# Optimization experiments

Measured on AMD Instinct MI355X. Metric: run time of the kernel, lower is better.

The kernel has to match this reference:

```python
import jax, jax.numpy as jnp
import numpy as np

N = 16000        # nodes
E = 256000       # edges
D_IN = 1280      # input node features
HID = 256        # hidden dim (all hidden_dims equal; required by res_linear shapes)
HEADS = 8
C = HID // HEADS # 32 channels per head
G = 32           # graphs in the batch
O = 64           # output labels (GO terms)
NB = 2           # conv blocks = len(hidden_dims) - 1
EPS = 1e-5


def _bn(h, g, b):
    # eval-mode BatchNorm1d with running_mean=0, running_var=1 (init state)
    return h * (g / jnp.sqrt(1.0 + EPS)) + b


def _seg_softmax(logits, seg, num):
    # numerically-stable segment softmax (PyG softmax semantics)
    m = jax.ops.segment_max(logits, seg, num_segments=num)
    e = jnp.exp(logits - m[seg])
    s = jax.ops.segment_sum(e, seg, num_segments=num)
    return e / (s[seg] + 1e-16)


def setup_inputs() -> dict:
    key = jax.random.key(0)
    ks = jax.random.split(key, 16)
    w = lambda i, sh: jax.random.normal(ks[i], sh, jnp.float32) * 0.05
    return {
        "x": jax.random.normal(ks[0], (N, D_IN), jnp.float32),
        "edge_index": jax.random.randint(ks[1], (2, E), 0, N),
        "batch": jnp.sort(jax.random.randint(ks[2], (N,), 0, G)),
        # feature_proj: Linear -> ReLU -> BN
        "fp_W": w(3, (D_IN, HID)), "fp_b": jnp.zeros(HID),
        "fp_g": jnp.ones(HID), "fp_be": jnp.zeros(HID),
        # GATv2Conv per block: lin_l, lin_r, att, out-bias
        "gat_Wl": w(4, (NB, HID, HID)), "gat_bl": jnp.zeros((NB, HID)),
        "gat_Wr": w(5, (NB, HID, HID)), "gat_br": jnp.zeros((NB, HID)),
        "gat_att": w(6, (NB, HEADS, C)), "gat_bias": jnp.zeros((NB, HID)),
        # GINConv MLP: Linear -> ReLU -> BN
        "gin_W": w(7, (NB, HID, HID)), "gin_b": jnp.zeros((NB, HID)),
        "gin_g": jnp.ones((NB, HID)), "gin_be": jnp.zeros((NB, HID)),
        # PyG LayerNorm (graph mode) affine
        "ln_g": jnp.ones((NB, HID)), "ln_b": jnp.zeros((NB, HID)),
        # residual linears
        "res_W": w(8, (NB, HID, HID)), "res_b": jnp.zeros((NB, HID)),
        # GlobalAttention gate MLP
        "pool_W1": w(9, (HID, HID)), "pool_b1": jnp.zeros(HID),
        "pool_W2": w(10, (HID, 1)), "pool_b2": jnp.zeros(1),
        # O label heads (hierarchy=None -> just the MLP), stacked
        "head_W1": w(11, (O, HID, 256)), "head_b1": jnp.zeros((O, 256)),
        "head_g": jnp.ones((O, 256)), "head_be": jnp.zeros((O, 256)),
        "head_W2": w(12, (O, 256)), "head_b2": jnp.zeros(O),
    }


def reference(x, edge_index, batch, fp_W, fp_b, fp_g, fp_be,
              gat_Wl, gat_bl, gat_Wr, gat_br, gat_att, gat_bias,
              gin_W, gin_b, gin_g, gin_be, ln_g, ln_b, res_W, res_b,
              pool_W1, pool_b1, pool_W2, pool_b2,
              head_W1, head_b1, head_g, head_be, head_W2, head_b2):
    n = x.shape[0]
    # feature_proj (eval: dropout = identity)
    h = _bn(jax.nn.relu(x @ fp_W + fp_b), fp_g, fp_be)

    src0, dst0 = edge_index[0], edge_index[1]
    loop = jnp.arange(n)
    src = jnp.concatenate([src0, loop])  # GATv2 adds self-loops by default
    dst = jnp.concatenate([dst0, loop])

    for i in range(NB):
        # ---- GATv2Conv (no activation after, per original control flow) ----
        xl = (h @ gat_Wl[i] + gat_bl[i]).reshape(n, HEADS, C)
        xr = (h @ gat_Wr[i] + gat_br[i]).reshape(n, HEADS, C)
        msg = xl[src]                                   # [E', H, C]
        eact = jax.nn.leaky_relu(msg + xr[dst], 0.2)
        logit = jnp.einsum('ehc,hc->eh', eact, gat_att[i])
        alpha = _seg_softmax(logit, dst, n)             # [E', H]
        h = jax.ops.segment_sum(alpha[:, :, None] * msg, dst,
                                num_segments=n).reshape(n, HID) + gat_bias[i]
        # ---- GINConv: nn((1+0)*x + sum_neighbors), then leaky_relu ----
        agg = jax.ops.segment_sum(h[src0], dst0, num_segments=n)
        gin = _bn(jax.nn.relu((h + agg) @ gin_W[i] + gin_b[i]), gin_g[i], gin_be[i])
        h = jax.nn.leaky_relu(gin, 0.2)
        # ---- PyG LayerNorm (graph mode, batch=None: global mean/std) + residual ----
        mu = h.mean()
        sd = jnp.std(h)
        ln = (h - mu) / (sd + EPS) * ln_g[i] + ln_b[i]
        h = jax.nn.leaky_relu(ln + (h @ res_W[i] + res_b[i]), 0.2)

    # ---- GlobalAttention pooling ----
    gate = jnp.tanh(h @ pool_W1 + pool_b1) @ pool_W2 + pool_b2   # [N, 1]
    a = _seg_softmax(gate[:, 0], batch, G)
    emb = jax.ops.segment_sum(a[:, None] * h, batch, num_segments=G)  # [G, HID]

    # ---- O label heads (hierarchy None -> MLP only), vectorized ----
    z = jnp.einsum('bd,odh->boh', emb, head_W1) + head_b1[None]
    z = _bn(jax.nn.silu(z), head_g[None], head_be[None])
    out = jnp.einsum('boh,oh->bo', z, head_W2) + head_b2[None]
    return out[:, :, None]  # torch.stack(outputs, dim=1) -> [G, O, 1]
```

## Files before the change

### kernel.cpp

```cpp
#include <hip/hip_runtime.h>
#include <math.h>

#define N_NODES 16000
#define N_EDGES 256000
#define EPE (N_EDGES + N_NODES)
#define DIN 1280
#define HID 256
#define HEADS 8
#define CPH 32
#define NG 32
#define NO 64
#define EPSC 1e-5f
#define CAP 32
#define XPAD 264
#define SPAD 40

typedef __bf16 bf16;
typedef __attribute__((ext_vector_type(8))) __bf16 bf16x8;
typedef __attribute__((ext_vector_type(4))) float floatx4;

__device__ __forceinline__ float lrelu(float v) { return v > 0.f ? v : 0.2f * v; }
__device__ __forceinline__ float bflo(unsigned int u) { return __uint_as_float(u << 16); }
__device__ __forceinline__ float bfhi(unsigned int u) { return __uint_as_float(u & 0xffff0000u); }

__global__ void wconv_gen(const float* __restrict__ W, bf16* __restrict__ Wt, int K, int total) {
    int idx = blockIdx.x * 256 + threadIdx.x;
    if (idx >= total) return;
    int per = K * HID;
    int l = idx / per, rem = idx - l * per;
    int n = rem / K, k = rem - n * K;
    Wt[idx] = (bf16)W[(size_t)l * per + (size_t)k * HID + n];
}

__global__ void wconv_pair(const float* __restrict__ Wl, const float* __restrict__ Wr,
                           bf16* __restrict__ Wt) {
    int idx = blockIdx.x * 256 + threadIdx.x;
    int n = idx >> 8, k = idx & 255;
    float v = (n < 256) ? Wl[(size_t)k * HID + n] : Wr[(size_t)k * HID + (n - 256)];
    Wt[idx] = (bf16)v;
}

__global__ __launch_bounds__(256) void gemm64(
    const bf16* __restrict__ A, const bf16* __restrict__ Bt,
    const float* __restrict__ bias, const float* __restrict__ bias2,
    bf16* __restrict__ C, int K, int ldc, int mode,
    const float* __restrict__ g, const float* __restrict__ be)
{
    __shared__ __align__(16) bf16 As[2][64 * SPAD];
    __shared__ __align__(16) bf16 Bs[2][64 * SPAD];
    const int tid = threadIdx.x;
    const int bm = blockIdx.y * 64, bn = blockIdx.x * 64;
    const int w = tid >> 6, lane = tid & 63;
    const int wm = w * 16;
    const int lrow = lane & 15, lk8 = (lane >> 4) * 8;
    const int row = tid >> 2, k8 = (tid & 3) * 8;

    const bf16* gA = A + (size_t)(bm + row) * K + k8;
    const bf16* gB = Bt + (size_t)(bn + row) * K + k8;

    floatx4 acc[4];
#pragma unroll
    for (int j = 0; j < 4; j++) acc[j] = (floatx4){0.f, 0.f, 0.f, 0.f};

    const int nk = K >> 5;
    bf16x8 ra = *(const bf16x8*)gA;
    bf16x8 rb = *(const bf16x8*)gB;

    for (int it = 0; it < nk; ++it) {
        int p = it & 1;
        *(bf16x8*)&As[p][row * SPAD + k8] = ra;
        *(bf16x8*)&Bs[p][row * SPAD + k8] = rb;
        __syncthreads();
        if (it + 1 < nk) {
            ra = *(const bf16x8*)(gA + (it + 1) * 32);
            rb = *(const bf16x8*)(gB + (it + 1) * 32);
        }
        bf16x8 af = *(const bf16x8*)&As[p][(wm + lrow) * SPAD + lk8];
        bf16x8 bfr[4];
#pragma unroll
        for (int j = 0; j < 4; j++) bfr[j] = *(const bf16x8*)&Bs[p][(16 * j + lrow) * SPAD + lk8];
#pragma unroll
        for (int j = 0; j < 4; j++)
            acc[j] = __builtin_amdgcn_mfma_f32_16x16x32_bf16(af, bfr[j], acc[j], 0, 0, 0);
    }

    const float inv = rsqrtf(1.f + EPSC);
    const int row0 = bm + wm + (lane >> 4) * 4;
#pragma unroll
    for (int j = 0; j < 4; j++) {
        int col = bn + 16 * j + lrow;
        float bcol = (col < HID) ? bias[col] : bias2[col - HID];
        float gc = (mode >= 1) ? g[col] * inv : 0.f;
        float bec = (mode >= 1) ? be[col] : 0.f;
#pragma unroll
        for (int r = 0; r < 4; r++) {
            float z = acc[j][r] + bcol;
            if (mode >= 1) { z = fmaxf(z, 0.f); z = z * gc + bec; }
            if (mode == 2) z = lrelu(z);
            C[(size_t)(row0 + r) * ldc + col] = (bf16)z;
        }
    }
}

__global__ __launch_bounds__(256, 1) void gemm_f32A(
    const float* __restrict__ A, const bf16* __restrict__ Bt,
    const float* __restrict__ bias, bf16* __restrict__ C, int K,
    const float* __restrict__ g, const float* __restrict__ be)
{
    __shared__ __align__(16) bf16 As[2][128 * SPAD];
    __shared__ __align__(16) bf16 Bs[2][128 * SPAD];
    const int tid = threadIdx.x;
    const int bm = blockIdx.y * 128, bn = blockIdx.x * 128;
    const int w = tid >> 6, lane = tid & 63;
    const int wm = (w & 1) * 64, wn = (w >> 1) * 64;
    const int lrow = lane & 15, lk8 = (lane >> 4) * 8;

    floatx4 acc[4][4];
#pragma unroll
    for (int i = 0; i < 4; i++)
#pragma unroll
        for (int j = 0; j < 4; j++) acc[i][j] = (floatx4){0.f, 0.f, 0.f, 0.f};

    const int r2 = tid >> 1, c2 = tid & 1;
    const float* gA = A + (size_t)(bm + r2) * K + c2 * 16;
    const bf16* gB = Bt + (size_t)(bn + r2) * K + c2 * 16;
    bf16* sA = &As[0][r2 * SPAD + c2 * 16];
    bf16* sB = &Bs[0][r2 * SPAD + c2 * 16];

    const int nk = K >> 5;
    float4 a[4][4];
    bf16x8 b[4][2];
#pragma unroll
    for (int u = 0; u < 4; u++) {
        const float* pa = gA + u * 32;
        a[u][0] = *(const float4*)(pa + 0);
        a[u][1] = *(const float4*)(pa + 4);
        a[u][2] = *(const float4*)(pa + 8);
        a[u][3] = *(const float4*)(pa + 12);
        const bf16* pb = gB + u * 32;
        b[u][0] = *(const bf16x8*)(pb + 0);
        b[u][1] = *(const bf16x8*)(pb + 8);
    }

    for (int it0 = 0; it0 < nk; it0 += 4) {
#pragma unroll
        for (int u = 0; u < 4; u++) {
            const int it = it0 + u;
            const int p = u & 1;
            const int po = p * 128 * SPAD;
            bf16x8 h0, h1;
            h0[0] = (bf16)a[u][0].x; h0[1] = (bf16)a[u][0].y; h0[2] = (bf16)a[u][0].z; h0[3] = (bf16)a[u][0].w;
            h0[4] = (bf16)a[u][1].x; h0[5] = (bf16)a[u][1].y; h0[6] = (bf16)a[u][1].z; h0[7] = (bf16)a[u][1].w;
            h1[0] = (bf16)a[u][2].x; h1[1] = (bf16)a[u][2].y; h1[2] = (bf16)a[u][2].z; h1[3] = (bf16)a[u][2].w;
            h1[4] = (bf16)a[u][3].x; h1[5] = (bf16)a[u][3].y; h1[6] = (bf16)a[u][3].z; h1[7] = (bf16)a[u][3].w;
            *(bf16x8*)(sA + po + 0) = h0;
            *(bf16x8*)(sA + po + 8) = h1;
            *(bf16x8*)(sB + po + 0) = b[u][0];
            *(bf16x8*)(sB + po + 8) = b[u][1];
            __syncthreads();
            if (it + 4 < nk) {
                const float* pa = gA + (it + 4) * 32;
                a[u][0] = *(const float4*)(pa + 0);
                a[u][1] = *(const float4*)(pa + 4);
                a[u][2] = *(const float4*)(pa + 8);
                a[u][3] = *(const float4*)(pa + 12);
                const bf16* pb = gB + (it + 4) * 32;
                b[u][0] = *(const bf16x8*)(pb + 0);
                b[u][1] = *(const bf16x8*)(pb + 8);
            }
            bf16x8 af[4], bfr[4];
#pragma unroll
            for (int i = 0; i < 4; i++) af[i] = *(const bf16x8*)&As[p][(wm + 16 * i + lrow) * SPAD + lk8];
#pragma unroll
            for (int j = 0; j < 4; j++) bfr[j] = *(const bf16x8*)&Bs[p][(wn + 16 * j + lrow) * SPAD + lk8];
#pragma unroll
            for (int i = 0; i < 4; i++)
#pragma unroll
                for (int j = 0; j < 4; j++)
                    acc[i][j] = __builtin_amdgcn_mfma_f32_16x16x32_bf16(af[i], bfr[j], acc[i][j], 0, 0, 0);
        }
    }

    const float inv = rsqrtf(1.f + EPSC);
#pragma unroll
    for (int j = 0; j < 4; j++) {
        int col = bn + wn + 16 * j + lrow;
        float bcol = bias[col];
        float gc = g[col] * inv;
        float bec = be[col];
#pragma unroll
        for (int i = 0; i < 4; i++) {
            int row0 = bm + wm + 16 * i + (lane >> 4) * 4;
#pragma unroll
            for (int r = 0; r < 4; r++) {
                float z = fmaxf(acc[i][j][r] + bcol, 0.f) * gc + bec;
                C[(size_t)(row0 + r) * HID + col] = (bf16)z;
            }
        }
    }
}

__global__ void hist_kernel(const int* __restrict__ ei, int* __restrict__ cnt) {
    int e = blockIdx.x * 256 + threadIdx.x;
    if (e >= EPE) return;
    int d = (e < N_EDGES) ? ei[N_EDGES + e] : (e - N_EDGES);
    atomicAdd(&cnt[d], 1);
}

__global__ __launch_bounds__(1024) void scan_kernel(const int* __restrict__ cnt,
                                                    int* __restrict__ roff, int* __restrict__ cursor) {
    __shared__ int wsum[16];
    int t = threadIdx.x;
    int base = t * 16;
    int local[16]; int s = 0;
#pragma unroll
    for (int i = 0; i < 16; i++) {
        int idx = base + i;
        int v = (idx < N_NODES) ? cnt[idx] : 0;
        local[i] = s; s += v;
    }
    int lane = t & 63, wid = t >> 6;
    int incl = s;
    for (int o = 1; o < 64; o <<= 1) { int v = __shfl_up(incl, o); if (lane >= o) incl += v; }
    if (lane == 63) wsum[wid] = incl;
    __syncthreads();
    if (t == 0) { int a = 0; for (int k = 0; k < 16; k++) { int v = wsum[k]; wsum[k] = a; a += v; } }
    __syncthreads();
    int texcl = incl - s + wsum[wid];
#pragma unroll
    for (int i = 0; i < 16; i++) {
        int idx = base + i;
        if (idx < N_NODES) { int o = texcl + local[i]; roff[idx] = o; cursor[idx] = o; }
    }
    if (t == 1023) roff[N_NODES] = texcl + s;
}

__global__ void scatter_kernel(const int* __restrict__ ei, int* __restrict__ cursor,
                               int* __restrict__ esrc) {
    int e = blockIdx.x * 256 + threadIdx.x;
    if (e >= EPE) return;
    int s, d;
    if (e < N_EDGES) { s = ei[e]; d = ei[N_EDGES + e]; }
    else { s = d = e - N_EDGES; }
    int pos = atomicAdd(&cursor[d], 1);
    esrc[pos] = s;
}

__global__ __launch_bounds__(256) void gat_fused(
    const bf16* __restrict__ XLR, const int* __restrict__ roff, const int* __restrict__ esrc,
    const float* __restrict__ att, const float* __restrict__ gbias, bf16* __restrict__ out)
{
    const int d = blockIdx.x, t = threadIdx.x;
    const int beg = roff[d], deg = roff[d + 1] - beg;
    __shared__ __align__(16) bf16 xs[CAP][XPAD];
    __shared__ __align__(16) float4 xa4[8 * 16];
    __shared__ float llog[CAP * 8];
    __shared__ float m_s[8], s_s[8], resc[8];

    if (t < 128) {
        int hh = t >> 4, cc = t & 15;
        int c = hh * 32 + cc * 2;
        float xr0 = (float)XLR[(size_t)d * 512 + 256 + c];
        float xr1 = (float)XLR[(size_t)d * 512 + 256 + c + 1];
        xa4[hh * 16 + cc] = (float4){xr0, att[c], xr1, att[c + 1]};
    }
    if (t < 8) { m_s[t] = -INFINITY; s_s[t] = 0.f; }

    const int jj = t & 31;
    const int hh = t >> 5;
    const int g = t >> 5, l = t & 31;
    float acc = 0.f;

    for (int c0 = 0; c0 < deg; c0 += CAP) {
        int cn = min(CAP, deg - c0);
        __syncthreads();
        for (int r = g; r < cn; r += 8) {
            int s = esrc[beg + c0 + r];
            *(bf16x8*)(&xs[r][l * 8]) = *(const bf16x8*)(XLR + (size_t)s * 512 + l * 8);
        }
        __syncthreads();
        if (jj < cn) {
            float lg = 0.f;
#pragma unroll
            for (int cc = 0; cc < 16; cc++) {
                int ce = (cc + jj) & 15;
                unsigned int p = *(const unsigned int*)&xs[jj][hh * 32 + ce * 2];
                float4 xa = xa4[hh * 16 + ce];
                lg += lrelu(bflo(p) + xa.x) * xa.y + lrelu(bfhi(p) + xa.z) * xa.w;
            }
            llog[jj * 8 + hh] = lg;
        }
        __syncthreads();
        if (t < 64) {
            int h2 = t & 7, j0 = t >> 3;
            float mx = -INFINITY;
            for (int j = j0; j < cn; j += 8) mx = fmaxf(mx, llog[j * 8 + h2]);
            for (int o = 8; o < 64; o <<= 1) mx = fmaxf(mx, __shfl_xor(mx, o));
            float mo = m_s[h2];
            float mn = fmaxf(mo, mx);
            float ss = 0.f;
            for (int j = j0; j < cn; j += 8) {
                float e = __expf(llog[j * 8 + h2] - mn);
                llog[j * 8 + h2] = e;
                ss += e;
            }
            for (int o = 8; o < 64; o <<= 1) ss += __shfl_xor(ss, o);
            if (t < 8) {
                float r = __expf(mo - mn);
                resc[h2] = r;
                s_s[h2] = s_s[h2] * r + ss;
                m_s[h2] = mn;
            }
        }
        __syncthreads();
        acc *= resc[hh];
        for (int j = 0; j < cn; j++)
            acc += llog[j * 8 + hh] * (float)xs[j][t];
    }
    out[(size_t)d * HID + t] = (bf16)(gbias[t] + acc / (s_s[hh] + 1e-16f));
}

__global__ __launch_bounds__(256) void gin_gather(
    const unsigned int* __restrict__ hu, const int* __restrict__ roff,
    const int* __restrict__ esrc, unsigned int* __restrict__ uu)
{
    int d = blockIdx.x, t = threadIdx.x;
    int grp = t >> 7, c = t & 127;
    int beg = roff[d], end = roff[d + 1];
    float a0 = 0.f, a1 = 0.f;
    int p = beg + grp;
    while (p + 14 < end) {
        int s[8];
#pragma unroll
        for (int k = 0; k < 8; k++) s[k] = esrc[p + 2 * k];
        unsigned int v[8];
#pragma unroll
        for (int k = 0; k < 8; k++) v[k] = hu[(size_t)s[k] * 128 + c];
#pragma unroll
        for (int k = 0; k < 8; k++) { a0 += bflo(v[k]); a1 += bfhi(v[k]); }
        p += 16;
    }
    for (; p < end; p += 2) {
        unsigned int v = hu[(size_t)esrc[p] * 128 + c];
        a0 += bflo(v); a1 += bfhi(v);
    }
    __shared__ float plo[128], phi[128];
    if (grp) { plo[c] = a0; phi[c] = a1; }
    __syncthreads();
    if (!grp) {
        a0 += plo[c]; a1 += phi[c];
        bf16 b0 = (bf16)a0, b1 = (bf16)a1;
        unsigned int r = ((unsigned int)*(unsigned short*)&b0) |
                         (((unsigned int)*(unsigned short*)&b1) << 16);
        uu[(size_t)d * 128 + c] = r;
    }
}

__global__ void stats_kernel(const bf16* __restrict__ x, float2* __restrict__ part, int n8) {
    float s = 0.f, sq = 0.f;
    for (int i = blockIdx.x * blockDim.x + threadIdx.x; i < n8; i += gridDim.x * blockDim.x) {
        bf16x8 v = *(const bf16x8*)(x + (size_t)i * 8);
#pragma unroll
        for (int j = 0; j < 8; j++) { float f = (float)v[j]; s += f; sq += f * f; }
    }
    for (int o = 32; o > 0; o >>= 1) { s += __shfl_down(s, o); sq += __shfl_down(sq, o); }
    __shared__ float ls[4], lq[4];
    int wid = threadIdx.x >> 6, lane = threadIdx.x & 63;
    if (lane == 0) { ls[wid] = s; lq[wid] = sq; }
    __syncthreads();
    if (threadIdx.x == 0)
        part[blockIdx.x] = make_float2(ls[0] + ls[1] + ls[2] + ls[3],
                                       lq[0] + lq[1] + lq[2] + lq[3]);
}

__global__ void stats_reduce(const float2* __restrict__ part, float* __restrict__ stat) {
    int t = threadIdx.x;
    float2 v = part[t];
    float s = v.x, q = v.y;
    for (int o = 32; o > 0; o >>= 1) { s += __shfl_down(s, o); q += __shfl_down(q, o); }
    __shared__ float ls[4], lq[4];
    int wid = t >> 6, lane = t & 63;
    if (lane == 0) { ls[wid] = s; lq[wid] = q; }
    __syncthreads();
    if (t == 0) { stat[0] = ls[0] + ls[1] + ls[2] + ls[3]; stat[1] = lq[0] + lq[1] + lq[2] + lq[3]; }
}

__global__ void ln_res_kernel(const bf16* __restrict__ h, const bf16* __restrict__ r,
                              const float* __restrict__ stats, const float* __restrict__ g,
                              const float* __restrict__ b, bf16* __restrict__ out)
{
    int i = (blockIdx.x * 256 + threadIdx.x) * 4;
    const float inv_n = 1.f / (float)((size_t)N_NODES * HID);
    float mu = stats[0] * inv_n;
    float var = stats[1] * inv_n - mu * mu;
    float sd = sqrtf(fmaxf(var, 0.f));
    float rs = 1.f / (sd + EPSC);
    int ch = i & (HID - 1);
#pragma unroll
    for (int j = 0; j < 4; j++) {
        float v = ((float)h[i + j] - mu) * rs * g[ch + j] + b[ch + j] + (float)r[i + j];
        out[i + j] = (bf16)lrelu(v);
    }
}

__global__ void gbound_kernel(const int* __restrict__ batch, int* __restrict__ gstart) {
    int g = threadIdx.x;
    if (g > NG) return;
    int lo = 0, hi = N_NODES;
    while (lo < hi) { int mid = (lo + hi) >> 1; if (batch[mid] < g) lo = mid + 1; else hi = mid; }
    gstart[g] = lo;
}

__global__ __launch_bounds__(256) void pool_gate_kernel(const bf16* __restrict__ t,
    const float* __restrict__ W2, const float* __restrict__ b2, float* __restrict__ gate)
{
    int n = blockIdx.x * 4 + (threadIdx.x >> 6);
    int lane = threadIdx.x & 63;
    const bf16* p = t + (size_t)n * HID + lane * 4;
    float4 w = *(const float4*)(W2 + lane * 4);
    float s = tanhf((float)p[0]) * w.x + tanhf((float)p[1]) * w.y
            + tanhf((float)p[2]) * w.z + tanhf((float)p[3]) * w.w;
    for (int o = 32; o > 0; o >>= 1) s += __shfl_down(s, o);
    if (lane == 0) gate[n] = s + b2[0];
}

__global__ __launch_bounds__(256) void pool_stats_kernel(
    float* __restrict__ gate, const int* __restrict__ gstart)
{
    int g = blockIdx.x, t = threadIdx.x;
    int lo = gstart[g], hi = gstart[g + 1];
    __shared__ float red[256];
    float m = -INFINITY;
    for (int n = lo + t; n < hi; n += 256) m = fmaxf(m, gate[n]);
    red[t] = m; __syncthreads();
    for (int st = 128; st > 0; st >>= 1) { if (t < st) red[t] = fmaxf(red[t], red[t + st]); __syncthreads(); }
    m = red[0]; __syncthreads();
    float s = 0.f;
    for (int n = lo + t; n < hi; n += 256) s += __expf(gate[n] - m);
    red[t] = s; __syncthreads();
    for (int st = 128; st > 0; st >>= 1) { if (t < st) red[t] += red[t + st]; __syncthreads(); }
    float sinv = 1.f / (red[0] + 1e-16f);
    for (int n = lo + t; n < hi; n += 256) gate[n] = __expf(gate[n] - m) * sinv;
}

__global__ __launch_bounds__(256) void emb_accum_kernel(
    const float* __restrict__ a, const int* __restrict__ batch,
    const bf16* __restrict__ h, float* __restrict__ emb)
{
    int n0 = blockIdx.x * 32, t = threadIdx.x;
    int cur = batch[n0]; float acc = 0.f;
    for (int j = 0; j < 32; j++) {
        int n = n0 + j;
        int b = batch[n];
        if (b != cur) { atomicAdd(&emb[cur * HID + t], acc); cur = b; acc = 0.f; }
        acc += a[n] * (float)h[(size_t)n * HID + t];
    }
    atomicAdd(&emb[cur * HID + t], acc);
}

__global__ __launch_bounds__(256) void heads_kernel(
    const float* __restrict__ emb, const float* __restrict__ W1, const float* __restrict__ b1,
    const float* __restrict__ hg, const float* __restrict__ hbe, const float* __restrict__ W2,
    const float* __restrict__ b2, float* __restrict__ out)
{
    int o = blockIdx.x;
    int g0 = blockIdx.y * 4;
    int k = threadIdx.x;
    __shared__ float se[4][HID];
    __shared__ float red[256];
#pragma unroll
    for (int j = 0; j < 4; j++) se[j][k] = emb[(g0 + j) * HID + k];
    __syncthreads();
    const float* w1p = W1 + (size_t)o * HID * HID + k;
    float zb = b1[o * HID + k];
    float z0 = zb, z1 = zb, z2 = zb, z3 = zb;
#pragma unroll 8
    for (int d = 0; d < HID; d++) {
        float w = w1p[(size_t)d * HID];
        z0 = fmaf(se[0][d], w, z0);
        z1 = fmaf(se[1][d], w, z1);
        z2 = fmaf(se[2][d], w, z2);
        z3 = fmaf(se[3][d], w, z3);
    }
    const float gk = hg[o * HID + k] * rsqrtf(1.f + EPSC);
    const float bek = hbe[o * HID + k];
    const float w2 = W2[o * HID + k];
    const float b2o = b2[o];
    float zz[4] = {z0, z1, z2, z3};
#pragma unroll
    for (int j = 0; j < 4; j++) {
        float z = zz[j];
        float sil = z / (1.f + expf(-z));
        red[k] = (sil * gk + bek) * w2;
        __syncthreads();
        for (int st = 128; st > 0; st >>= 1) { if (k < st) red[k] += red[k + st]; __syncthreads(); }
        if (k == 0) out[(g0 + j) * NO + o] = red[0] + b2o;
        __syncthreads();
    }
}

extern "C" void kernel_launch(void* const* d_in, const int* in_sizes, int n_in,
                              void* d_out, int out_size, void* d_ws, size_t ws_size,
                              hipStream_t stream) {
    const float* x        = (const float*)d_in[0];
    const int*   ei       = (const int*)  d_in[1];
    const int*   batch    = (const int*)  d_in[2];
    const float* fp_W     = (const float*)d_in[3];
    const float* fp_b     = (const float*)d_in[4];
    const float* fp_g     = (const float*)d_in[5];
    const float* fp_be    = (const float*)d_in[6];
    const float* gat_Wl   = (const float*)d_in[7];
    const float* gat_bl   = (const float*)d_in[8];
    const float* gat_Wr   = (const float*)d_in[9];
    const float* gat_br   = (const float*)d_in[10];
    const float* gat_att  = (const float*)d_in[11];
    const float* gat_bias = (const float*)d_in[12];
    const float* gin_W    = (const float*)d_in[13];
    const float* gin_b    = (const float*)d_in[14];
    const float* gin_g    = (const float*)d_in[15];
    const float* gin_be   = (const float*)d_in[16];
    const float* ln_g     = (const float*)d_in[17];
    const float* ln_b     = (const float*)d_in[18];
    const float* res_W    = (const float*)d_in[19];
    const float* res_b    = (const float*)d_in[20];
    const float* pool_W1  = (const float*)d_in[21];
    const float* pool_b1  = (const float*)d_in[22];
    const float* pool_W2  = (const float*)d_in[23];
    const float* pool_b2  = (const float*)d_in[24];
    const float* head_W1  = (const float*)d_in[25];
    const float* head_b1  = (const float*)d_in[26];
    const float* head_g   = (const float*)d_in[27];
    const float* head_be  = (const float*)d_in[28];
    const float* head_W2  = (const float*)d_in[29];
    const float* head_b2  = (const float*)d_in[30];
    float* out = (float*)d_out;

    char* base = (char*)d_ws;
    size_t off = 0;
    auto alloc = [&](size_t bytes) -> char* {
        char* p = base + off; off += (bytes + 255) & ~(size_t)255; return p;
    };
    int*   esrc   = (int*)  alloc((size_t)EPE * 4);
    int*   cnt    = (int*)  alloc((size_t)N_NODES * 4);
    int*   roff   = (int*)  alloc((size_t)(N_NODES + 1) * 4);
    int*   cursor = (int*)  alloc((size_t)N_NODES * 4);
    float* gate   = (float*)alloc((size_t)N_NODES * 4);
    int*   gstart = (int*)  alloc((NG + 1) * 4);
    float* emb    = (float*)alloc(NG * HID * 4);
    float* stat   = (float*)alloc(8);
    float2* statp = (float2*)alloc(256 * 8);
    bf16*  Hb0    = (bf16*) alloc((size_t)N_NODES * HID * 2);
    bf16*  Hb1    = (bf16*) alloc((size_t)N_NODES * HID * 2);
    bf16*  XLR    = (bf16*) alloc((size_t)N_NODES * 512 * 2);
    bf16*  fpWt   = (bf16*) alloc((size_t)DIN * HID * 2);
    bf16*  wlrT0  = (bf16*) alloc((size_t)512 * HID * 2);
    bf16*  wlrT1  = (bf16*) alloc((size_t)512 * HID * 2);
    bf16*  gwT    = (bf16*) alloc((size_t)2 * HID * HID * 2);
    bf16*  rwT    = (bf16*) alloc((size_t)2 * HID * HID * 2);
    bf16*  pwT    = (bf16*) alloc((size_t)HID * HID * 2);
    bf16*  Ub     = XLR;
    bf16*  wlrT[2] = { wlrT0, wlrT1 };

    wconv_gen<<<(DIN * HID + 255) / 256, 256, 0, stream>>>(fp_W, fpWt, DIN, DIN * HID);
    wconv_pair<<<512, 256, 0, stream>>>(gat_Wl, gat_Wr, wlrT0);
    wconv_pair<<<512, 256, 0, stream>>>(gat_Wl + HID * HID, gat_Wr + HID * HID, wlrT1);
    wconv_gen<<<512, 256, 0, stream>>>(gin_W, gwT, HID, 2 * HID * HID);
    wconv_gen<<<512, 256, 0, stream>>>(res_W, rwT, HID, 2 * HID * HID);
    wconv_gen<<<256, 256, 0, stream>>>(pool_W1, pwT, HID, HID * HID);

    hipMemsetAsync(cnt, 0, N_NODES * sizeof(int), stream);
    hist_kernel<<<(EPE + 255) / 256, 256, 0, stream>>>(ei, cnt);
    scan_kernel<<<1, 1024, 0, stream>>>(cnt, roff, cursor);
    scatter_kernel<<<(EPE + 255) / 256, 256, 0, stream>>>(ei, cursor, esrc);
    gbound_kernel<<<1, 64, 0, stream>>>(batch, gstart);

    dim3 gridF(2, 125);
    dim3 g64_256(4, 250);
    dim3 g64_512(8, 250);
    gemm_f32A<<<gridF, 256, 0, stream>>>(x, fpWt, fp_b, Hb0, DIN, fp_g, fp_be);

    for (int i = 0; i < 2; i++) {
        gemm64<<<g64_512, 256, 0, stream>>>(Hb0, wlrT[i], gat_bl + i * HID, gat_br + i * HID,
                                            XLR, HID, 512, 0, nullptr, nullptr);
        gat_fused<<<N_NODES, 256, 0, stream>>>(XLR, roff, esrc, gat_att + i * HEADS * CPH,
                                               gat_bias + i * HID, Hb1);
        gin_gather<<<N_NODES, 256, 0, stream>>>((const unsigned int*)Hb1, roff, esrc,
                                                (unsigned int*)Ub);
        gemm64<<<g64_256, 256, 0, stream>>>(Ub, gwT + (size_t)i * HID * HID, gin_b + i * HID,
                                            nullptr, Hb0, HID, HID, 2,
                                            gin_g + i * HID, gin_be + i * HID);
        stats_kernel<<<256, 256, 0, stream>>>(Hb0, statp, (N_NODES * HID) / 8);
        stats_reduce<<<1, 256, 0, stream>>>(statp, stat);
        gemm64<<<g64_256, 256, 0, stream>>>(Hb0, rwT + (size_t)i * HID * HID, res_b + i * HID,
                                            nullptr, Hb1, HID, HID, 0, nullptr, nullptr);
        ln_res_kernel<<<(N_NODES * HID) / 1024, 256, 0, stream>>>(Hb0, Hb1, stat,
                                                                  ln_g + i * HID, ln_b + i * HID, Hb0);
    }

    gemm64<<<g64_256, 256, 0, stream>>>(Hb0, pwT, pool_b1, nullptr, Hb1, HID, HID, 0, nullptr, nullptr);
    pool_gate_kernel<<<N_NODES / 4, 256, 0, stream>>>(Hb1, pool_W2, pool_b2, gate);
    pool_stats_kernel<<<NG, 256, 0, stream>>>(gate, gstart);
    hipMemsetAsync(emb, 0, NG * HID * sizeof(float), stream);
    emb_accum_kernel<<<N_NODES / 32, 256, 0, stream>>>(gate, batch, Hb0, emb);

    dim3 hgrid(NO, 8);
    heads_kernel<<<hgrid, 256, 0, stream>>>(emb, head_W1, head_b1, head_g, head_be,
                                            head_W2, head_b2, out);
}
```

Before: 608.4 us.

## Fuse LayerNorm stats and residual epilogue into GEMMs, rework GAT aggregation

```diff
diff --git a/kernel.cpp b/kernel.cpp
--- a/kernel.cpp
+++ b/kernel.cpp
@@ -22,6 +22,10 @@
 __device__ __forceinline__ float lrelu(float v) { return v > 0.f ? v : 0.2f * v; }
 __device__ __forceinline__ float bflo(unsigned int u) { return __uint_as_float(u << 16); }
 __device__ __forceinline__ float bfhi(unsigned int u) { return __uint_as_float(u & 0xffff0000u); }
+__device__ __forceinline__ unsigned int bfpack(float x, float y) {
+    bf16 b0 = (bf16)x, b1 = (bf16)y;
+    return ((unsigned int)*(unsigned short*)&b0) | (((unsigned int)*(unsigned short*)&b1) << 16);
+}
 
 __global__ void wconv_gen(const float* __restrict__ W, bf16* __restrict__ Wt, int K, int total) {
     int idx = blockIdx.x * 256 + threadIdx.x;
@@ -44,7 +48,8 @@
     const bf16* __restrict__ A, const bf16* __restrict__ Bt,
     const float* __restrict__ bias, const float* __restrict__ bias2,
     bf16* __restrict__ C, int K, int ldc, int mode,
-    const float* __restrict__ g, const float* __restrict__ be)
+    const float* __restrict__ g, const float* __restrict__ be,
+    float2* __restrict__ statp, const float* __restrict__ stat)
 {
     __shared__ __align__(16) bf16 As[2][64 * SPAD];
     __shared__ __align__(16) bf16 Bs[2][64 * SPAD];
@@ -86,19 +91,46 @@
 
     const float inv = rsqrtf(1.f + EPSC);
     const int row0 = bm + wm + (lane >> 4) * 4;
+    float mu = 0.f, rs = 0.f;
+    if (mode == 3) {
+        const float inv_n = 1.f / (float)((size_t)N_NODES * HID);
+        mu = stat[0] * inv_n;
+        float var = stat[1] * inv_n - mu * mu;
+        rs = 1.f / (sqrtf(fmaxf(var, 0.f)) + EPSC);
+    }
+    float sz = 0.f, sq = 0.f;
 #pragma unroll
     for (int j = 0; j < 4; j++) {
         int col = bn + 16 * j + lrow;
         float bcol = (col < HID) ? bias[col] : bias2[col - HID];
-        float gc = (mode >= 1) ? g[col] * inv : 0.f;
-        float bec = (mode >= 1) ? be[col] : 0.f;
+        float gc = (mode >= 2) ? g[col] : 0.f;
+        float bec = (mode >= 2) ? be[col] : 0.f;
 #pragma unroll
         for (int r = 0; r < 4; r++) {
             float z = acc[j][r] + bcol;
-            if (mode >= 1) { z = fmaxf(z, 0.f); z = z * gc + bec; }
-            if (mode == 2) z = lrelu(z);
+            if (mode == 2) {
+                z = fmaxf(z, 0.f) * (gc * inv) + bec;
+                z = lrelu(z);
+                sz += z; sq += z * z;
+            } else if (mode == 3) {
+                float h = (float)A[(size_t)(row0 + r) * K + col];
+                z = (h - mu) * rs * gc + bec + z;
+                z = lrelu(z);
+            }
             C[(size_t)(row0 + r) * ldc + col] = (bf16)z;
         }
+    }
+    if (mode == 2) {
+        for (int o = 32; o > 0; o >>= 1) { sz += __shfl_down(sz, o); sq += __shfl_down(sq, o); }
+        __syncthreads();
+        float* rs_ = (float*)&As[0][0];
+        float* rq_ = (float*)&Bs[0][0];
+        if (lane == 0) { rs_[w] = sz; rq_[w] = sq; }
+        __syncthreads();
+        if (tid == 0)
+            statp[blockIdx.y * gridDim.x + blockIdx.x] =
+                make_float2(rs_[0] + rs_[1] + rs_[2] + rs_[3],
+                            rq_[0] + rq_[1] + rq_[2] + rq_[3]);
     }
 }
 
@@ -208,7 +240,9 @@
 }
 
 __global__ __launch_bounds__(1024) void scan_kernel(const int* __restrict__ cnt,
-                                                    int* __restrict__ roff, int* __restrict__ cursor) {
+                                                    int* __restrict__ roff, int* __restrict__ cursor,
+                                                    const int* __restrict__ batch,
+                                                    int* __restrict__ gstart) {
     __shared__ int wsum[16];
     int t = threadIdx.x;
     int base = t * 16;
@@ -233,6 +267,11 @@
         if (idx < N_NODES) { int o = texcl + local[i]; roff[idx] = o; cursor[idx] = o; }
     }
     if (t == 1023) roff[N_NODES] = texcl + s;
+    if (t <= NG) {
+        int lo = 0, hi = N_NODES;
+        while (lo < hi) { int mid = (lo + hi) >> 1; if (batch[mid] < t) lo = mid + 1; else hi = mid; }
+        gstart[t] = lo;
+    }
 }
 
 __global__ void scatter_kernel(const int* __restrict__ ei, int* __restrict__ cursor,
@@ -255,6 +294,7 @@
     __shared__ __align__(16) bf16 xs[CAP][XPAD];
     __shared__ __align__(16) float4 xa4[8 * 16];
     __shared__ float llog[CAP * 8];
+    __shared__ float comb[256];
     __shared__ float m_s[8], s_s[8], resc[8];
 
     if (t < 128) {
@@ -268,15 +308,19 @@
 
     const int jj = t & 31;
     const int hh = t >> 5;
-    const int g = t >> 5, l = t & 31;
-    float acc = 0.f;
+    const int sg = t >> 5, sl = t & 31;
+    const int half = t >> 7;
+    const int tc = t & 127;
+    const int ch0 = tc * 2;
+    const int ha = tc >> 4;
+    float a0 = 0.f, a1 = 0.f;
 
     for (int c0 = 0; c0 < deg; c0 += CAP) {
         int cn = min(CAP, deg - c0);
         __syncthreads();
-        for (int r = g; r < cn; r += 8) {
+        for (int r = sg; r < cn; r += 8) {
             int s = esrc[beg + c0 + r];
-            *(bf16x8*)(&xs[r][l * 8]) = *(const bf16x8*)(XLR + (size_t)s * 512 + l * 8);
+            *(bf16x8*)(&xs[r][sl * 8]) = *(const bf16x8*)(XLR + (size_t)s * 512 + sl * 8);
         }
         __syncthreads();
         if (jj < cn) {
@@ -313,11 +357,24 @@
             }
         }
         __syncthreads();
-        acc *= resc[hh];
-        for (int j = 0; j < cn; j++)
-            acc += llog[j * 8 + hh] * (float)xs[j][t];
-    }
-    out[(size_t)d * HID + t] = (bf16)(gbias[t] + acc / (s_s[hh] + 1e-16f));
+        float rsf = resc[ha];
+        a0 *= rsf; a1 *= rsf;
+        for (int j = half; j < cn; j += 2) {
+            float wgt = llog[j * 8 + ha];
+            unsigned int p = *(const unsigned int*)&xs[j][ch0];
+            a0 = fmaf(wgt, bflo(p), a0);
+            a1 = fmaf(wgt, bfhi(p), a1);
+        }
+    }
+    __syncthreads();
+    if (half) { comb[ch0] = a0; comb[ch0 + 1] = a1; }
+    __syncthreads();
+    if (!half) {
+        float r = 1.f / (s_s[ha] + 1e-16f);
+        float v0 = gbias[ch0] + (a0 + comb[ch0]) * r;
+        float v1 = gbias[ch0 + 1] + (a1 + comb[ch0 + 1]) * r;
+        *(unsigned int*)(out + (size_t)d * HID + ch0) = bfpack(v0, v1);
+    }
 }
 
 __global__ __launch_bounds__(256) void gin_gather(
@@ -349,66 +406,20 @@
     __syncthreads();
     if (!grp) {
         a0 += plo[c]; a1 += phi[c];
-        bf16 b0 = (bf16)a0, b1 = (bf16)a1;
-        unsigned int r = ((unsigned int)*(unsigned short*)&b0) |
-                         (((unsigned int)*(unsigned short*)&b1) << 16);
-        uu[(size_t)d * 128 + c] = r;
-    }
-}
-
-__global__ void stats_kernel(const bf16* __restrict__ x, float2* __restrict__ part, int n8) {
-    float s = 0.f, sq = 0.f;
-    for (int i = blockIdx.x * blockDim.x + threadIdx.x; i < n8; i += gridDim.x * blockDim.x) {
-        bf16x8 v = *(const bf16x8*)(x + (size_t)i * 8);
-#pragma unroll
-        for (int j = 0; j < 8; j++) { float f = (float)v[j]; s += f; sq += f * f; }
-    }
-    for (int o = 32; o > 0; o >>= 1) { s += __shfl_down(s, o); sq += __shfl_down(sq, o); }
-    __shared__ float ls[4], lq[4];
-    int wid = threadIdx.x >> 6, lane = threadIdx.x & 63;
-    if (lane == 0) { ls[wid] = s; lq[wid] = sq; }
-    __syncthreads();
-    if (threadIdx.x == 0)
-        part[blockIdx.x] = make_float2(ls[0] + ls[1] + ls[2] + ls[3],
-                                       lq[0] + lq[1] + lq[2] + lq[3]);
-}
-
-__global__ void stats_reduce(const float2* __restrict__ part, float* __restrict__ stat) {
+        uu[(size_t)d * 128 + c] = bfpack(a0, a1);
+    }
+}
+
+__global__ void stats_reduce(const float2* __restrict__ part, float* __restrict__ stat, int n) {
     int t = threadIdx.x;
-    float2 v = part[t];
-    float s = v.x, q = v.y;
+    float s = 0.f, q = 0.f;
+    for (int i = t; i < n; i += 256) { float2 v = part[i]; s += v.x; q += v.y; }
     for (int o = 32; o > 0; o >>= 1) { s += __shfl_down(s, o); q += __shfl_down(q, o); }
     __shared__ float ls[4], lq[4];
     int wid = t >> 6, lane = t & 63;
     if (lane == 0) { ls[wid] = s; lq[wid] = q; }
     __syncthreads();
     if (t == 0) { stat[0] = ls[0] + ls[1] + ls[2] + ls[3]; stat[1] = lq[0] + lq[1] + lq[2] + lq[3]; }
-}
-
-__global__ void ln_res_kernel(const bf16* __restrict__ h, const bf16* __restrict__ r,
-                              const float* __restrict__ stats, const float* __restrict__ g,
-                              const float* __restrict__ b, bf16* __restrict__ out)
-{
-    int i = (blockIdx.x * 256 + threadIdx.x) * 4;
-    const float inv_n = 1.f / (float)((size_t)N_NODES * HID);
-    float mu = stats[0] * inv_n;
-    float var = stats[1] * inv_n - mu * mu;
-    float sd = sqrtf(fmaxf(var, 0.f));
-    float rs = 1.f / (sd + EPSC);
-    int ch = i & (HID - 1);
-#pragma unroll
-    for (int j = 0; j < 4; j++) {
-        float v = ((float)h[i + j] - mu) * rs * g[ch + j] + b[ch + j] + (float)r[i + j];
-        out[i + j] = (bf16)lrelu(v);
-    }
-}
-
-__global__ void gbound_kernel(const int* __restrict__ batch, int* __restrict__ gstart) {
-    int g = threadIdx.x;
-    if (g > NG) return;
-    int lo = 0, hi = N_NODES;
-    while (lo < hi) { int mid = (lo + hi) >> 1; if (batch[mid] < g) lo = mid + 1; else hi = mid; }
-    gstart[g] = lo;
 }
 
 __global__ __launch_bounds__(256) void pool_gate_kernel(const bf16* __restrict__ t,
@@ -548,7 +559,7 @@
     int*   gstart = (int*)  alloc((NG + 1) * 4);
     float* emb    = (float*)alloc(NG * HID * 4);
     float* stat   = (float*)alloc(8);
-    float2* statp = (float2*)alloc(256 * 8);
+    float2* statp = (float2*)alloc(1024 * 8);
     bf16*  Hb0    = (bf16*) alloc((size_t)N_NODES * HID * 2);
     bf16*  Hb1    = (bf16*) alloc((size_t)N_NODES * HID * 2);
     bf16*  XLR    = (bf16*) alloc((size_t)N_NODES * 512 * 2);
@@ -570,38 +581,39 @@
 
     hipMemsetAsync(cnt, 0, N_NODES * sizeof(int), stream);
     hist_kernel<<<(EPE + 255) / 256, 256, 0, stream>>>(ei, cnt);
-    scan_kernel<<<1, 1024, 0, stream>>>(cnt, roff, cursor);
+    scan_kernel<<<1, 1024, 0, stream>>>(cnt, roff, cursor, batch, gstart);
     scatter_kernel<<<(EPE + 255) / 256, 256, 0, stream>>>(ei, cursor, esrc);
-    gbound_kernel<<<1, 64, 0, stream>>>(batch, gstart);
 
     dim3 gridF(2, 125);
     dim3 g64_256(4, 250);
     dim3 g64_512(8, 250);
     gemm_f32A<<<gridF, 256, 0, stream>>>(x, fpWt, fp_b, Hb0, DIN, fp_g, fp_be);
 
+    bf16* hcur = Hb0;
+    bf16* hoth = Hb1;
     for (int i = 0; i < 2; i++) {
-        gemm64<<<g64_512, 256, 0, stream>>>(Hb0, wlrT[i], gat_bl + i * HID, gat_br + i * HID,
-                                            XLR, HID, 512, 0, nullptr, nullptr);
+        gemm64<<<g64_512, 256, 0, stream>>>(hcur, wlrT[i], gat_bl + i * HID, gat_br + i * HID,
+                                            XLR, HID, 512, 0, nullptr, nullptr, nullptr, nullptr);
         gat_fused<<<N_NODES, 256, 0, stream>>>(XLR, roff, esrc, gat_att + i * HEADS * CPH,
-                                               gat_bias + i * HID, Hb1);
-        gin_gather<<<N_NODES, 256, 0, stream>>>((const unsigned int*)Hb1, roff, esrc,
+                                               gat_bias + i * HID, hoth);
+        gin_gather<<<N_NODES, 256, 0, stream>>>((const unsigned int*)hoth, roff, esrc,
                                                 (unsigned int*)Ub);
         gemm64<<<g64_256, 256, 0, stream>>>(Ub, gwT + (size_t)i * HID * HID, gin_b + i * HID,
-                                            nullptr, Hb0, HID, HID, 2,
-                                            gin_g + i * HID, gin_be + i * HID);
-        stats_kernel<<<256, 256, 0, stream>>>(Hb0, statp, (N_NODES * HID) / 8);
-        stats_reduce<<<1, 256, 0, stream>>>(statp, stat);
-        gemm64<<<g64_256, 256, 0, stream>>>(Hb0, rwT + (size_t)i * HID * HID, res_b + i * HID,
-                                            nullptr, Hb1, HID, HID, 0, nullptr, nullptr);
-        ln_res_kernel<<<(N_NODES * HID) / 1024, 256, 0, stream>>>(Hb0, Hb1, stat,
-                                                                  ln_g + i * HID, ln_b + i * HID, Hb0);
-    }
-
-    gemm64<<<g64_256, 256, 0, stream>>>(Hb0, pwT, pool_b1, nullptr, Hb1, HID, HID, 0, nullptr, nullptr);
-    pool_gate_kernel<<<N_NODES / 4, 256, 0, stream>>>(Hb1, pool_W2, pool_b2, gate);
+                                            nullptr, hcur, HID, HID, 2,
+                                            gin_g + i * HID, gin_be + i * HID, statp, nullptr);
+        stats_reduce<<<1, 256, 0, stream>>>(statp, stat, 1000);
+        gemm64<<<g64_256, 256, 0, stream>>>(hcur, rwT + (size_t)i * HID * HID, res_b + i * HID,
+                                            nullptr, hoth, HID, HID, 3,
+                                            ln_g + i * HID, ln_b + i * HID, nullptr, stat);
+        bf16* tmp = hcur; hcur = hoth; hoth = tmp;
+    }
+
+    gemm64<<<g64_256, 256, 0, stream>>>(hcur, pwT, pool_b1, nullptr, hoth, HID, HID, 0,
+                                        nullptr, nullptr, nullptr, nullptr);
+    pool_gate_kernel<<<N_NODES / 4, 256, 0, stream>>>(hoth, pool_W2, pool_b2, gate);
     pool_stats_kernel<<<NG, 256, 0, stream>>>(gate, gstart);
     hipMemsetAsync(emb, 0, NG * HID * sizeof(float), stream);
-    emb_accum_kernel<<<N_NODES / 32, 256, 0, stream>>>(gate, batch, Hb0, emb);
+    emb_accum_kernel<<<N_NODES / 32, 256, 0, stream>>>(gate, batch, hcur, emb);
 
     dim3 hgrid(NO, 8);
     heads_kernel<<<hgrid, 256, 0, stream>>>(emb, head_W1, head_b1, head_g, head_be,
```

After: 593.8 us. 2.4% less time.
